# Performance work log

Measured on AMD Instinct MI355X. Metric: run time of the kernel, lower is better.

Reference implementation:

```python
import jax, jax.numpy as jnp
import numpy as np
from itertools import product


def _gen_exps(num_vars, degree):
    return [e for e in product(range(degree + 1), repeat=num_vars) if sum(e) <= degree]

EXP_W = _gen_exps(7, 3)  # 120 terms
EXP_B = _gen_exps(3, 3)  # 20 terms
EXP_M = _gen_exps(5, 3)  # 56 terms (+1 diagonal coeff)


def _powers(x, exps):
    return {e: x ** e for e in exps}


def setup_inputs() -> dict:
    key = jax.random.key(0)
    ks = jax.random.split(key, 12)
    B, Din, Dout = 65536, 64, 64
    return {
        'x1': jax.random.normal(ks[0], (B, Din), jnp.float32),
        's1': jax.random.normal(ks[1], (B, Dout), jnp.float32),
        'y1': jax.random.normal(ks[2], (B, Dout), jnp.float32),
        'x2': jax.random.normal(ks[3], (B, Din), jnp.float32),
        's2': jax.random.normal(ks[4], (B, Dout), jnp.float32),
        'y2': jax.random.normal(ks[5], (B, Dout), jnp.float32),
        'w': jax.random.normal(ks[6], (Dout, Din), jnp.float32) * 0.1,
        'b': jax.random.normal(ks[7], (Dout,), jnp.float32) * 0.1,
        'm': jax.random.normal(ks[8], (Dout, Dout), jnp.float32) * 0.1,
        'params_w': jax.random.normal(ks[9], (len(EXP_W),), jnp.float32) * 0.1,
        'params_b': jax.random.normal(ks[10], (len(EXP_B),), jnp.float32) * 0.1,
        'params_m': jax.random.normal(ks[11], (len(EXP_M) + 1,), jnp.float32) * 0.1,
    }


def _dw(x1, s1, y1, x2, s2, y2, w, params_w):
    px1 = _powers(x1, {e[0] for e in EXP_W})
    ps1 = _powers(s1, {e[1] for e in EXP_W})
    py1 = _powers(y1, {e[2] for e in EXP_W})
    px2 = _powers(x2, {e[3] for e in EXP_W})
    ps2 = _powers(s2, {e[4] for e in EXP_W})
    py2 = _powers(y2, {e[5] for e in EXP_W})
    pw = _powers(w, {e[6] for e in EXP_W})
    inv_b = 1.0 / x1.shape[0]
    delta_w = jnp.zeros_like(w)
    for i, e in enumerate(EXP_W):
        y_term = ps1[e[1]] * py1[e[2]] * ps2[e[4]] * py2[e[5]]  # [B, Dout]
        x_term = px1[e[0]] * px2[e[3]]                          # [B, Din]
        delta_w = delta_w + (params_w[i] * inv_b) * (y_term.T @ x_term) * pw[e[6]]
    return delta_w  # bound=None (identity), l2_reg=0


def _db(y1, y2, b, params_b):
    py1 = _powers(y1, {e[0] for e in EXP_B})
    py2 = _powers(y2, {e[1] for e in EXP_B})
    pb = _powers(b, {e[2] for e in EXP_B})
    inv_b = 1.0 / y1.shape[0]
    delta_b = jnp.zeros_like(b)
    for i, e in enumerate(EXP_B):
        delta_b = delta_b + (params_b[i] * inv_b) * jnp.sum(py1[e[0]] * py2[e[1]], axis=0) * pb[e[2]]
    return delta_b


def _dm(y1, y2, m, params_m):
    ey1 = {e[0] for e in EXP_M} | {e[1] for e in EXP_M}
    ey2 = {e[2] for e in EXP_M} | {e[3] for e in EXP_M}
    py1 = _powers(y1, ey1)
    py2 = _powers(y2, ey2)
    pm = _powers(m, {e[4] for e in EXP_M})
    inv_b = 1.0 / y1.shape[0]
    delta_m = jnp.zeros_like(m)
    for i, e in enumerate(EXP_M):
        left = py1[e[1]] * py2[e[3]]   # [B, Dout]
        right = py1[e[0]] * py2[e[2]]  # [B, Dout]
        delta_m = delta_m + (params_m[i] * inv_b) * (left.T @ right) * pm[e[4]]
    delta_m = delta_m + params_m[-1] * jnp.eye(m.shape[0], dtype=m.dtype)
    return delta_m


def reference(x1, s1, y1, x2, s2, y2, w, b, m, params_w, params_b, params_m):
    delta_w = _dw(x1, s1, y1, x2, s2, y2, w, params_w)
    delta_b = _db(y1, y2, b, params_b)
    delta_m = _dm(y1, y2, m, params_m)
    return delta_w, delta_b, delta_m
```

## Files before the change

kernel.cpp:

```cpp
#include <hip/hip_runtime.h>
#include <type_traits>
#include <stdint.h>

#define DEV __device__ __forceinline__

typedef float f32x4 __attribute__((ext_vector_type(4)));
typedef short bf16x8 __attribute__((ext_vector_type(8)));
typedef unsigned short u16;
typedef u16 u16x4 __attribute__((ext_vector_type(4)));

static constexpr int BTOT = 65536;
static constexpr int KB   = 64;
static constexpr int NCHT = BTOT / KB;
static constexpr int NG   = 56;
static constexpr int NCOLSUM = 45;
static constexpr float INVB = 1.0f / (float)BTOT;

static constexpr int NWIN  = 32;
static constexpr int CHW   = NCHT / NWIN;
static constexpr int NCOLG = 7;
static constexpr int GRID  = 8*NWIN;
static constexpr int BUFHALF = 8*4096;

struct Col {
  int nslot, np;
  int8_t sexp[8][6];
  int8_t pa[8], pb[8];
  int16_t gout[8];
  uint8_t ldmask;
};

struct Tables {
  int nW, nB, nM, nA, nX;
  int8_t expw[120][7];
  int8_t expb[20][3];
  int8_t expm[56][5];
  int8_t am[35][4];
  int8_t xm[10][2];
  Col col[NCOLG];
  int8_t wtype[120]; int16_t widx[120]; int8_t wpow[120];
  int8_t mtype[56];  int16_t midx[56];  int8_t mpow[56];
  int16_t bcol[20];  int8_t bpow[20];
  int err, gcount;
};

constexpr int aidf(const Tables& t,int a,int b,int c,int d){
  for(int i=0;i<t.nA;i++)
    if(t.am[i][0]==a&&t.am[i][1]==b&&t.am[i][2]==c&&t.am[i][3]==d) return i;
  return -1;
}
constexpr int xidf(const Tables& t,int a,int b){
  for(int i=0;i<t.nX;i++) if(t.xm[i][0]==a&&t.xm[i][1]==b) return i;
  return -1;
}

constexpr Tables makeTables(){
  Tables t{};
  t.err = 0;
  t.nW=0;
  for(int e0=0;e0<4;e0++)for(int e1=0;e1<4;e1++)for(int e2=0;e2<4;e2++)
  for(int e3=0;e3<4;e3++)for(int e4=0;e4<4;e4++)for(int e5=0;e5<4;e5++)
  for(int e6=0;e6<4;e6++) if(e0+e1+e2+e3+e4+e5+e6<=3){
    t.expw[t.nW][0]=(int8_t)e0; t.expw[t.nW][1]=(int8_t)e1; t.expw[t.nW][2]=(int8_t)e2;
    t.expw[t.nW][3]=(int8_t)e3; t.expw[t.nW][4]=(int8_t)e4; t.expw[t.nW][5]=(int8_t)e5;
    t.expw[t.nW][6]=(int8_t)e6; t.nW++;
  }
  t.nB=0;
  for(int e0=0;e0<4;e0++)for(int e1=0;e1<4;e1++)for(int e2=0;e2<4;e2++)
    if(e0+e1+e2<=3){ t.expb[t.nB][0]=(int8_t)e0; t.expb[t.nB][1]=(int8_t)e1; t.expb[t.nB][2]=(int8_t)e2; t.nB++; }
  t.nM=0;
  for(int e0=0;e0<4;e0++)for(int e1=0;e1<4;e1++)for(int e2=0;e2<4;e2++)
  for(int e3=0;e3<4;e3++)for(int e4=0;e4<4;e4++)
    if(e0+e1+e2+e3+e4<=3){
      t.expm[t.nM][0]=(int8_t)e0; t.expm[t.nM][1]=(int8_t)e1; t.expm[t.nM][2]=(int8_t)e2;
      t.expm[t.nM][3]=(int8_t)e3; t.expm[t.nM][4]=(int8_t)e4; t.nM++;
    }
  t.nA=0;
  for(int a=0;a<4;a++)for(int b=0;b<4;b++)for(int c=0;c<4;c++)for(int d=0;d<4;d++)
    if(a+b+c+d<=3){ t.am[t.nA][0]=(int8_t)a; t.am[t.nA][1]=(int8_t)b; t.am[t.nA][2]=(int8_t)c; t.am[t.nA][3]=(int8_t)d; t.nA++; }
  t.nX=0;
  for(int a=0;a<4;a++)for(int b=0;b<4;b++)
    if(a+b<=3){ t.xm[t.nX][0]=(int8_t)a; t.xm[t.nX][1]=(int8_t)b; t.nX++; }

  int wslot[35][10]; int mslot[10][10];
  for(int i=0;i<35;i++)for(int j=0;j<10;j++) wslot[i][j]=-1;
  for(int i=0;i<10;i++)for(int j=0;j<10;j++) mslot[i][j]=-1;

  int slot=0;

  {
    Col& c=t.col[0]; c.nslot=4; c.np=8;
    int ym[4][2]={{0,1},{1,0},{0,2},{1,1}};
    for(int s=0;s<4;s++){ for(int q=0;q<6;q++)c.sexp[s][q]=0;
      c.sexp[s][1]=(int8_t)ym[s][0]; c.sexp[s][3]=(int8_t)ym[s][1]; }
    int p=0;
    for(int L=0;L<2;L++)for(int R=0;R<4;R++){
      c.pa[p]=(int8_t)L; c.pb[p]=(int8_t)R; c.gout[p]=(int16_t)slot;
      mslot[xidf(t,ym[L][0],ym[L][1])][xidf(t,ym[R][0],ym[R][1])]=slot; slot++; p++;
    }
  }
  {
    Col& c=t.col[1]; c.nslot=5; c.np=8;
    int ym[5][2]={{0,1},{1,0},{0,2},{1,1},{2,0}};
    for(int s=0;s<5;s++){ for(int q=0;q<6;q++)c.sexp[s][q]=0;
      c.sexp[s][1]=(int8_t)ym[s][0]; c.sexp[s][3]=(int8_t)ym[s][1]; }
    int p=0;
    for(int L=0;L<2;L++){
      c.pa[p]=(int8_t)L; c.pb[p]=4; c.gout[p]=(int16_t)slot;
      mslot[xidf(t,ym[L][0],ym[L][1])][xidf(t,2,0)]=slot; slot++; p++;
    }
    for(int i=0;i<3;i++)for(int j=0;j<2;j++){
      c.pa[p]=(int8_t)(2+i); c.pb[p]=(int8_t)j; c.gout[p]=(int16_t)slot;
      mslot[xidf(t,ym[2+i][0],ym[2+i][1])][xidf(t,ym[j][0],ym[j][1])]=slot; slot++; p++;
    }
  }
  for(int wc=0; wc<2; wc++){
    Col& c=t.col[2+2*wc]; c.nslot=6; c.np=8;
    int am2[2][2]={{1,0},{0,1}};
    int xb[4][2]={{0,1},{1,0},{0,2},{1,1}};
    for(int s=0;s<6;s++) for(int q=0;q<6;q++) c.sexp[s][q]=0;
    for(int s=0;s<2;s++){
      c.sexp[s][wc?2:0]=(int8_t)am2[s][0]; c.sexp[s][wc?3:1]=(int8_t)am2[s][1];
    }
    for(int s=0;s<4;s++){ c.sexp[2+s][4]=(int8_t)xb[s][0]; c.sexp[2+s][5]=(int8_t)xb[s][1]; }
    int p=0;
    for(int a=0;a<2;a++)for(int b=0;b<4;b++){
      int amid = wc? aidf(t,0,0,am2[a][0],am2[a][1]) : aidf(t,am2[a][0],am2[a][1],0,0);
      if(amid<0) t.err+=1;
      c.pa[p]=(int8_t)a; c.pb[p]=(int8_t)(2+b); c.gout[p]=(int16_t)slot;
      wslot[amid][xidf(t,xb[b][0],xb[b][1])]=slot; slot++; p++;
    }
  }
  for(int wc=0; wc<2; wc++){
    Col& c=t.col[3+2*wc]; c.nslot=8; c.np=8;
    int am5[5][2]={{1,0},{0,1},{2,0},{1,1},{0,2}};
    int xb[3][2]={{2,0},{0,1},{1,0}};
    for(int s=0;s<8;s++) for(int q=0;q<6;q++) c.sexp[s][q]=0;
    for(int s=0;s<5;s++){
      c.sexp[s][wc?2:0]=(int8_t)am5[s][0]; c.sexp[s][wc?3:1]=(int8_t)am5[s][1];
    }
    for(int s=0;s<3;s++){ c.sexp[5+s][4]=(int8_t)xb[s][0]; c.sexp[5+s][5]=(int8_t)xb[s][1]; }
    int p=0;
    for(int a=0;a<2;a++){
      int amid = wc? aidf(t,0,0,am5[a][0],am5[a][1]) : aidf(t,am5[a][0],am5[a][1],0,0);
      if(amid<0) t.err+=1;
      c.pa[p]=(int8_t)a; c.pb[p]=5; c.gout[p]=(int16_t)slot;
      wslot[amid][xidf(t,2,0)]=slot; slot++; p++;
    }
    for(int i=0;i<3;i++)for(int j=0;j<2;j++){
      int amid = wc? aidf(t,0,0,am5[2+i][0],am5[2+i][1]) : aidf(t,am5[2+i][0],am5[2+i][1],0,0);
      if(amid<0) t.err+=1;
      c.pa[p]=(int8_t)(2+i); c.pb[p]=(int8_t)(6+j); c.gout[p]=(int16_t)slot;
      wslot[amid][xidf(t,xb[1+j][0],xb[1+j][1])]=slot; slot++; p++;
    }
  }
  {
    Col& c=t.col[6]; c.nslot=6; c.np=8;
    int a4[4][4]={{1,0,1,0},{1,0,0,1},{0,1,1,0},{0,1,0,1}};
    int xb[2][2]={{0,1},{1,0}};
    for(int s=0;s<6;s++) for(int q=0;q<6;q++) c.sexp[s][q]=0;
    for(int s=0;s<4;s++) for(int q=0;q<4;q++) c.sexp[s][q]=(int8_t)a4[s][q];
    for(int s=0;s<2;s++){ c.sexp[4+s][4]=(int8_t)xb[s][0]; c.sexp[4+s][5]=(int8_t)xb[s][1]; }
    int p=0;
    for(int a=0;a<4;a++)for(int b=0;b<2;b++){
      int amid = aidf(t,a4[a][0],a4[a][1],a4[a][2],a4[a][3]);
      if(amid<0) t.err+=1;
      c.pa[p]=(int8_t)a; c.pb[p]=(int8_t)(4+b); c.gout[p]=(int16_t)slot;
      wslot[amid][xidf(t,xb[b][0],xb[b][1])]=slot; slot++; p++;
    }
  }
  t.gcount=slot;
  if(slot!=NG) t.err+=1;

  for(int ci=0; ci<NCOLG; ci++){
    unsigned m=0;
    for(int s=0;s<t.col[ci].nslot;s++)
      for(int v=0;v<6;v++) if(t.col[ci].sexp[s][v]>0) m |= (1u<<v);
    t.col[ci].ldmask=(uint8_t)m;
  }

  for(int i=0;i<t.nW;i++){
    const int8_t* e=t.expw[i];
    bool u0=(e[0]==0&&e[3]==0);
    bool v0=(e[1]==0&&e[2]==0&&e[4]==0&&e[5]==0);
    t.wpow[i]=e[6];
    if(u0){ t.wtype[i]=1; t.widx[i]=(int16_t)aidf(t,e[1],e[2],e[4],e[5]); }
    else if(v0){ t.wtype[i]=2; t.widx[i]=(int16_t)xidf(t,e[0],e[3]); }
    else {
      int s=wslot[aidf(t,e[1],e[2],e[4],e[5])][xidf(t,e[0],e[3])];
      if(s<0) t.err+=1;
      t.wtype[i]=0; t.widx[i]=(int16_t)s;
    }
  }
  for(int i=0;i<t.nM;i++){
    const int8_t* e=t.expm[i];
    bool L0=(e[1]==0&&e[3]==0), R0=(e[0]==0&&e[2]==0);
    t.mpow[i]=e[4];
    if(L0){ t.mtype[i]=2; t.midx[i]=(int16_t)aidf(t,0,e[0],0,e[2]); }
    else if(R0){ t.mtype[i]=1; t.midx[i]=(int16_t)aidf(t,0,e[1],0,e[3]); }
    else {
      int s=mslot[xidf(t,e[1],e[3])][xidf(t,e[0],e[2])];
      if(s<0) t.err+=1;
      t.mtype[i]=0; t.midx[i]=(int16_t)s;
    }
  }
  for(int i=0;i<t.nB;i++){
    const int8_t* e=t.expb[i];
    t.bcol[i]=(int16_t)aidf(t,0,e[0],0,e[1]); t.bpow[i]=e[2];
  }
  return t;
}

constexpr Tables TB = makeTables();
static_assert(TB.err==0 && TB.gcount==56, "table build failed");
static_assert(TB.nW==120 && TB.nB==20 && TB.nM==56 && TB.nA==35 && TB.nX==10, "enumeration mismatch");

template<int N, typename F>
DEV void sunroll(F&& f){
  if constexpr (N > 0){
    sunroll<N-1>(static_cast<F&&>(f));
    f(std::integral_constant<int, N-1>{});
  }
}
template<int E> DEV float ipw(float x){
  if constexpr(E==0) return 1.0f;
  else if constexpr(E==1) return x;
  else if constexpr(E==2) return x*x;
  else return x*x*x;
}
DEV u16 f2bf(float f){
  uint32_t u = __builtin_bit_cast(uint32_t, f);
  u = u + 0x7FFFu + ((u>>16)&1u);
  return (u16)(u>>16);
}

DEV bf16x8 readFrag(const u16* L, int slot, int sb, int tt, int l){
  return *(const bf16x8*)&L[slot*4096 + ((sb*4 + tt)*64 + l)*8];
}
DEV f32x4 mfma_(bf16x8 a, bf16x8 b, f32x4 c){
  return __builtin_amdgcn_mfma_f32_16x16x32_bf16(a, b, c, 0, 0, 0);
}

template<int CI>
DEV void colGemm(const float* __restrict__ s1,const float* __restrict__ y1,
                 const float* __restrict__ s2,const float* __restrict__ y2,
                 const float* __restrict__ x1,const float* __restrict__ x2,
                 float* __restrict__ G, u16* lds, int tid, int bi)
{
  constexpr int NS = TB.col[CI].nslot;
  constexpr unsigned LM = TB.col[CI].ldmask;

  const int l = tid&63, w = tid>>6;
  const int wbase = ((w>>3)*4 + (l>>4))*512 + (((w>>1)&3)*16 + (l&15))*8 + (w&1)*4;

  const int c0 = bi*CHW, c1 = c0+CHW;
  f32x4 acc[4][2] = {};
  float rw[6][4] = {};

  auto issue = [&](int ck){
    const int b0 = (ck*KB + w*4)*64 + l;
    #pragma unroll
    for(int j=0;j<4;j++){
      const int off = b0 + j*64;
      if constexpr(LM&1u)  rw[0][j]=s1[off];
      if constexpr(LM&2u)  rw[1][j]=y1[off];
      if constexpr(LM&4u)  rw[2][j]=s2[off];
      if constexpr(LM&8u)  rw[3][j]=y2[off];
      if constexpr(LM&16u) rw[4][j]=x1[off];
      if constexpr(LM&32u) rw[5][j]=x2[off];
    }
  };
  auto stage = [&](int buf){
    u16* L = lds + buf*BUFHALF;
    sunroll<NS>([&](auto S){
      constexpr int s = decltype(S)::value;
      u16x4 o4;
      #pragma unroll
      for(int j=0;j<4;j++){
        float v = ipw<TB.col[CI].sexp[s][0]>(rw[0][j])
                * ipw<TB.col[CI].sexp[s][1]>(rw[1][j])
                * ipw<TB.col[CI].sexp[s][2]>(rw[2][j])
                * ipw<TB.col[CI].sexp[s][3]>(rw[3][j])
                * ipw<TB.col[CI].sexp[s][4]>(rw[4][j])
                * ipw<TB.col[CI].sexp[s][5]>(rw[5][j]);
        o4[j]=f2bf(v);
      }
      *(u16x4*)&L[s*4096 + wbase] = o4;
    });
  };

  issue(c0);
  stage(0);
  asm volatile("s_waitcnt lgkmcnt(0)" ::: "memory");
  __builtin_amdgcn_s_barrier();
  __builtin_amdgcn_sched_barrier(0);

  for(int k=c0; k<c1; ++k){
    const int t = k - c0;
    const bool notlast = (k+1 < c1);
    if(notlast) issue(k+1);

    const u16* L = lds + (t&1)*BUFHALF;
    sunroll<16>([&](auto WW){
      constexpr int ww = decltype(WW)::value;
      if(w==ww){
        constexpr int p  = ww>>1;
        constexpr int SA = TB.col[CI].pa[p];
        constexpr int SB = TB.col[CI].pb[p];
        constexpr int DB = (ww&1)*2;
        #pragma unroll
        for(int sb=0; sb<2; ++sb){
          bf16x8 Af[4];
          #pragma unroll
          for(int o2=0;o2<4;o2++) Af[o2]=readFrag(L,SA,sb,o2,l);
          #pragma unroll
          for(int dd=0;dd<2;dd++){
            bf16x8 Bf=readFrag(L,SB,sb,DB+dd,l);
            #pragma unroll
            for(int o2=0;o2<4;o2++) acc[o2][dd]=mfma_(Af[o2],Bf,acc[o2][dd]);
          }
        }
      }
    });

    if(notlast) stage((t+1)&1);

    asm volatile("s_waitcnt lgkmcnt(0)" ::: "memory");
    __builtin_amdgcn_s_barrier();
    __builtin_amdgcn_sched_barrier(0);
  }

  const int r0=(l>>4)*4, cc=l&15;
  sunroll<16>([&](auto WW){
    constexpr int ww = decltype(WW)::value;
    if(w==ww){
      constexpr int p  = ww>>1;
      constexpr int GS = TB.col[CI].gout[p];
      constexpr int DB = (ww&1)*2;
      float* dst = G + GS*4096;
      #pragma unroll
      for(int o2=0;o2<4;o2++)
        #pragma unroll
        for(int dd=0;dd<2;dd++)
          #pragma unroll
          for(int r=0;r<4;r++)
            atomicAdd(&dst[(o2*16+r0+r)*64 + (DB+dd)*16+cc], acc[o2][dd][r]);
    }
  });
}

DEV void colRed(const float* __restrict__ s1,const float* __restrict__ y1,
                const float* __restrict__ s2,const float* __restrict__ y2,
                const float* __restrict__ x1,const float* __restrict__ x2,
                float* __restrict__ col, float* ldsF, int tid, int bi)
{
  const int ch=tid&63, g16=tid>>6;
  const int base = bi*2048;
  float accv[45];
  sunroll<45>([&](auto K){ accv[decltype(K)::value]=0.f; });
  for(int r=base+g16; r<base+2048; r+=16){
    const int off=r*64+ch;
    const float v0=s1[off],v1=y1[off],v2=s2[off],v3=y2[off],v4=x1[off],v5=x2[off];
    sunroll<35>([&](auto K){
      constexpr int k=decltype(K)::value;
      accv[k] += ipw<TB.am[k][0]>(v0)*ipw<TB.am[k][1]>(v1)*ipw<TB.am[k][2]>(v2)*ipw<TB.am[k][3]>(v3);
    });
    sunroll<10>([&](auto K){
      constexpr int k=decltype(K)::value;
      accv[35+k] += ipw<TB.xm[k][0]>(v4)*ipw<TB.xm[k][1]>(v5);
    });
  }
  sunroll<6>([&](auto RR){
    constexpr int rr=decltype(RR)::value;
    __syncthreads();
    sunroll<8>([&](auto Q){
      constexpr int q=decltype(Q)::value;
      if constexpr(rr*8+q < 45)
        ldsF[(q*16+g16)*64+ch]=accv[rr*8+q];
    });
    __syncthreads();
    {
      const int k=tid>>6, c=tid&63;
      const int idx=rr*8+k;
      if(k<8 && idx<45){
        float s=0.f;
        #pragma unroll
        for(int gg=0; gg<16; gg++) s+=ldsF[(k*16+gg)*64+c];
        atomicAdd(&col[idx*64+c], s);
      }
    }
  });
}

__global__ __launch_bounds__(1024, 4) void k_main(
    const float* __restrict__ x1, const float* __restrict__ s1, const float* __restrict__ y1,
    const float* __restrict__ x2, const float* __restrict__ s2, const float* __restrict__ y2,
    float* __restrict__ G, float* __restrict__ col)
{
  __shared__ u16 lds[2*BUFHALF];
  const int tid = threadIdx.x;
  const int u = blockIdx.x >> 5;
  const int g = blockIdx.x & 31;
  if      (u==0) colGemm<0>(s1,y1,s2,y2,x1,x2,G,lds,tid,g);
  else if (u==1) colGemm<1>(s1,y1,s2,y2,x1,x2,G,lds,tid,g);
  else if (u==2) colGemm<2>(s1,y1,s2,y2,x1,x2,G,lds,tid,g);
  else if (u==3) colGemm<3>(s1,y1,s2,y2,x1,x2,G,lds,tid,g);
  else if (u==4) colGemm<4>(s1,y1,s2,y2,x1,x2,G,lds,tid,g);
  else if (u==5) colGemm<5>(s1,y1,s2,y2,x1,x2,G,lds,tid,g);
  else if (u==6) colGemm<6>(s1,y1,s2,y2,x1,x2,G,lds,tid,g);
  else           colRed(s1,y1,s2,y2,x1,x2,col,(float*)lds,tid,g);
}

__global__ __launch_bounds__(256) void k_combine(
    const float* __restrict__ G, const float* __restrict__ col,
    const float* __restrict__ w, const float* __restrict__ b, const float* __restrict__ m,
    const float* __restrict__ parw, const float* __restrict__ parb, const float* __restrict__ parm,
    float* __restrict__ out)
{
  const int n = blockIdx.x*256 + threadIdx.x;
  const int o = n>>6, d = n&63;
  const float wv = w[n], mv = m[n];
  const float wp[4] = {1.f, wv, wv*wv, wv*wv*wv};
  const float mp[4] = {1.f, mv, mv*mv, mv*mv*mv};
  float aw=0.f, am=0.f;
  sunroll<120>([&](auto II){
    constexpr int i = decltype(II)::value;
    constexpr int ty = TB.wtype[i];
    constexpr int ix = TB.widx[i];
    constexpr int q  = TB.wpow[i];
    float val;
    if constexpr(ty==0) val = G[ix*4096 + n];
    else if constexpr(ty==1) val = col[ix*64 + o];
    else val = col[(35+ix)*64 + d];
    aw += parw[i] * val * wp[q];
  });
  sunroll<56>([&](auto II){
    constexpr int i = decltype(II)::value;
    constexpr int ty = TB.mtype[i];
    constexpr int ix = TB.midx[i];
    constexpr int q  = TB.mpow[i];
    float val;
    if constexpr(ty==0) val = G[ix*4096 + n];
    else if constexpr(ty==1) val = col[ix*64 + o];
    else val = col[ix*64 + d];
    am += parm[i] * val * mp[q];
  });
  aw *= INVB; am *= INVB;
  if (o==d) am += parm[56];
  out[n] = aw;
  out[4160 + n] = am;
  if (n < 64){
    const float bv = b[n];
    const float bp[4] = {1.f, bv, bv*bv, bv*bv*bv};
    float ab=0.f;
    sunroll<20>([&](auto II){
      constexpr int i = decltype(II)::value;
      constexpr int cix = TB.bcol[i];
      constexpr int q = TB.bpow[i];
      ab += parb[i] * col[cix*64 + n] * bp[q];
    });
    out[4096 + n] = ab * INVB;
  }
}

extern "C" void kernel_launch(void* const* d_in, const int* in_sizes, int n_in,
                              void* d_out, int out_size, void* d_ws, size_t ws_size,
                              hipStream_t stream)
{
  const float* x1=(const float*)d_in[0];
  const float* s1=(const float*)d_in[1];
  const float* y1=(const float*)d_in[2];
  const float* x2=(const float*)d_in[3];
  const float* s2=(const float*)d_in[4];
  const float* y2=(const float*)d_in[5];
  const float* w =(const float*)d_in[6];
  const float* b =(const float*)d_in[7];
  const float* m =(const float*)d_in[8];
  const float* parw=(const float*)d_in[9];
  const float* parb=(const float*)d_in[10];
  const float* parm=(const float*)d_in[11];

  float* G   = (float*)d_ws;
  float* col = G + NG*4096;

  hipMemsetAsync(d_ws, 0, (size_t)(NG*4096 + NCOLSUM*64)*sizeof(float), stream);
  k_main<<<GRID, 1024, 0, stream>>>(x1,s1,y1,x2,s2,y2,G,col);
  k_combine<<<16, 256, 0, stream>>>(G,col,w,b,m,parw,parb,parm,(float*)d_out);
}
```

Measured before the change: 97.11 us.

## Warp-specialize column GEMM into producer and MFMA consumer wavefronts

Splits the 16 wavefronts into 8 producers, which load inputs, compute the power products and write bf16 tiles to LDS, and 8 consumers, which run the MFMA chain for one full 64x64 product each. The consumers raise their scheduling priority. Previously every wave did both jobs in lockstep. The split aims to overlap global loads and elementwise work with the matrix math, and each consumer now owns a whole output tile. The cost is that each consumer holds a larger accumulator, 16 f32x4, which raises register pressure. Half the waves also never use the MFMA units, so throughput depends on the two groups staying balanced across barriers.

```diff
diff --git a/kernel.cpp b/kernel.cpp
--- a/kernel.cpp
+++ b/kernel.cpp
@@ -7,7 +7,7 @@
 typedef float f32x4 __attribute__((ext_vector_type(4)));
 typedef short bf16x8 __attribute__((ext_vector_type(8)));
 typedef unsigned short u16;
-typedef u16 u16x4 __attribute__((ext_vector_type(4)));
+typedef u16 u16x8 __attribute__((ext_vector_type(8)));
 
 static constexpr int BTOT = 65536;
 static constexpr int KB   = 64;
@@ -251,102 +251,102 @@
   constexpr unsigned LM = TB.col[CI].ldmask;
 
   const int l = tid&63, w = tid>>6;
-  const int wbase = ((w>>3)*4 + (l>>4))*512 + (((w>>1)&3)*16 + (l&15))*8 + (w&1)*4;
-
   const int c0 = bi*CHW, c1 = c0+CHW;
-  f32x4 acc[4][2] = {};
-  float rw[6][4] = {};
-
-  auto issue = [&](int ck){
-    const int b0 = (ck*KB + w*4)*64 + l;
-    #pragma unroll
-    for(int j=0;j<4;j++){
-      const int off = b0 + j*64;
-      if constexpr(LM&1u)  rw[0][j]=s1[off];
-      if constexpr(LM&2u)  rw[1][j]=y1[off];
-      if constexpr(LM&4u)  rw[2][j]=s2[off];
-      if constexpr(LM&8u)  rw[3][j]=y2[off];
-      if constexpr(LM&16u) rw[4][j]=x1[off];
-      if constexpr(LM&32u) rw[5][j]=x2[off];
-    }
-  };
-  auto stage = [&](int buf){
-    u16* L = lds + buf*BUFHALF;
-    sunroll<NS>([&](auto S){
-      constexpr int s = decltype(S)::value;
-      u16x4 o4;
+
+  if (w < 8){
+    const int pw = w;
+    const int wrbase = ((pw>>2)*4 + (l>>4))*512 + ((pw&3)*16 + (l&15))*8;
+    float rw[6][8];
+
+    auto LOAD = [&](int ck){
+      const int b0 = (ck*KB + pw*8)*64 + l;
       #pragma unroll
-      for(int j=0;j<4;j++){
-        float v = ipw<TB.col[CI].sexp[s][0]>(rw[0][j])
-                * ipw<TB.col[CI].sexp[s][1]>(rw[1][j])
-                * ipw<TB.col[CI].sexp[s][2]>(rw[2][j])
-                * ipw<TB.col[CI].sexp[s][3]>(rw[3][j])
-                * ipw<TB.col[CI].sexp[s][4]>(rw[4][j])
-                * ipw<TB.col[CI].sexp[s][5]>(rw[5][j]);
-        o4[j]=f2bf(v);
+      for(int j=0;j<8;j++){
+        const int off = b0 + j*64;
+        if constexpr(LM&1u)  rw[0][j]=s1[off];
+        if constexpr(LM&2u)  rw[1][j]=y1[off];
+        if constexpr(LM&4u)  rw[2][j]=s2[off];
+        if constexpr(LM&8u)  rw[3][j]=y2[off];
+        if constexpr(LM&16u) rw[4][j]=x1[off];
+        if constexpr(LM&32u) rw[5][j]=x2[off];
       }
-      *(u16x4*)&L[s*4096 + wbase] = o4;
-    });
-  };
-
-  issue(c0);
-  stage(0);
-  asm volatile("s_waitcnt lgkmcnt(0)" ::: "memory");
-  __builtin_amdgcn_s_barrier();
-  __builtin_amdgcn_sched_barrier(0);
-
-  for(int k=c0; k<c1; ++k){
-    const int t = k - c0;
-    const bool notlast = (k+1 < c1);
-    if(notlast) issue(k+1);
-
-    const u16* L = lds + (t&1)*BUFHALF;
-    sunroll<16>([&](auto WW){
-      constexpr int ww = decltype(WW)::value;
-      if(w==ww){
-        constexpr int p  = ww>>1;
-        constexpr int SA = TB.col[CI].pa[p];
-        constexpr int SB = TB.col[CI].pb[p];
-        constexpr int DB = (ww&1)*2;
+    };
+    auto PROD = [&](int buf){
+      u16* L = lds + buf*BUFHALF;
+      sunroll<NS>([&](auto S){
+        constexpr int s = decltype(S)::value;
+        u16x8 o8;
         #pragma unroll
-        for(int sb=0; sb<2; ++sb){
-          bf16x8 Af[4];
-          #pragma unroll
-          for(int o2=0;o2<4;o2++) Af[o2]=readFrag(L,SA,sb,o2,l);
-          #pragma unroll
-          for(int dd=0;dd<2;dd++){
-            bf16x8 Bf=readFrag(L,SB,sb,DB+dd,l);
-            #pragma unroll
-            for(int o2=0;o2<4;o2++) acc[o2][dd]=mfma_(Af[o2],Bf,acc[o2][dd]);
-          }
+        for(int j=0;j<8;j++){
+          float v = ipw<TB.col[CI].sexp[s][0]>(rw[0][j])
+                  * ipw<TB.col[CI].sexp[s][1]>(rw[1][j])
+                  * ipw<TB.col[CI].sexp[s][2]>(rw[2][j])
+                  * ipw<TB.col[CI].sexp[s][3]>(rw[3][j])
+                  * ipw<TB.col[CI].sexp[s][4]>(rw[4][j])
+                  * ipw<TB.col[CI].sexp[s][5]>(rw[5][j]);
+          o8[j]=f2bf(v);
         }
-      }
-    });
-
-    if(notlast) stage((t+1)&1);
-
+        *(u16x8*)&L[s*4096 + wrbase] = o8;
+      });
+    };
+
+    LOAD(c0); PROD(c0&1);
     asm volatile("s_waitcnt lgkmcnt(0)" ::: "memory");
     __builtin_amdgcn_s_barrier();
     __builtin_amdgcn_sched_barrier(0);
-  }
-
-  const int r0=(l>>4)*4, cc=l&15;
-  sunroll<16>([&](auto WW){
-    constexpr int ww = decltype(WW)::value;
-    if(w==ww){
-      constexpr int p  = ww>>1;
-      constexpr int GS = TB.col[CI].gout[p];
-      constexpr int DB = (ww&1)*2;
-      float* dst = G + GS*4096;
+
+    for(int k=c0; k<c1; ++k){
+      if(k+1 < c1){ LOAD(k+1); PROD((k+1)&1); }
+      asm volatile("s_waitcnt lgkmcnt(0)" ::: "memory");
+      __builtin_amdgcn_s_barrier();
+      __builtin_amdgcn_sched_barrier(0);
+    }
+  } else {
+    int aslot=0, bslot=0, gsl=0;
+    sunroll<8>([&](auto PP){
+      constexpr int p = decltype(PP)::value;
+      if(w == 8+p){
+        aslot = TB.col[CI].pa[p];
+        bslot = TB.col[CI].pb[p];
+        gsl   = TB.col[CI].gout[p];
+      }
+    });
+    f32x4 acc[4][4] = {};
+
+    __builtin_amdgcn_s_barrier();
+    __builtin_amdgcn_sched_barrier(0);
+
+    for(int k=c0; k<c1; ++k){
+      const u16* L = lds + (k&1)*BUFHALF;
+      __builtin_amdgcn_s_setprio(1);
       #pragma unroll
-      for(int o2=0;o2<4;o2++)
+      for(int sb=0; sb<2; ++sb){
+        bf16x8 Af[4];
         #pragma unroll
-        for(int dd=0;dd<2;dd++)
+        for(int o2=0;o2<4;o2++) Af[o2]=readFrag(L,aslot,sb,o2,l);
+        #pragma unroll
+        for(int dd=0;dd<4;dd++){
+          bf16x8 Bf=readFrag(L,bslot,sb,dd,l);
           #pragma unroll
-          for(int r=0;r<4;r++)
-            atomicAdd(&dst[(o2*16+r0+r)*64 + (DB+dd)*16+cc], acc[o2][dd][r]);
-    }
-  });
+          for(int o2=0;o2<4;o2++) acc[o2][dd]=mfma_(Af[o2],Bf,acc[o2][dd]);
+        }
+      }
+      __builtin_amdgcn_s_setprio(0);
+      asm volatile("s_waitcnt lgkmcnt(0)" ::: "memory");
+      __builtin_amdgcn_s_barrier();
+      __builtin_amdgcn_sched_barrier(0);
+    }
+
+    const int r0=(l>>4)*4, cc=l&15;
+    float* dst = G + gsl*4096;
+    #pragma unroll
+    for(int o2=0;o2<4;o2++)
+      #pragma unroll
+      for(int dd=0;dd<4;dd++)
+        #pragma unroll
+        for(int r=0;r<4;r++)
+          atomicAdd(&dst[(o2*16+r0+r)*64 + dd*16+cc], acc[o2][dd][r]);
+  }
 }
 
 DEV void colRed(const float* __restrict__ s1,const float* __restrict__ y1,
```

Result: slower. 107.7 us (+10.9%).

## Remap staging thread-to-element layout and replace per-wave unrolled dispatch with runtime slots

Applied to the files above, without the earlier changes.

Each thread now loads a different (channel, batch) element from global memory and writes its packed bf16 values contiguously at tid*4 in LDS, so the LDS stores are linear. The fragment layout read by MFMA is unchanged. The 16-way compile-time per-wave branch, in both the MFMA loop and the atomic epilogue, is replaced by runtime slot indices chosen once. This shrinks code size and instruction-cache pressure. The cost is less coalesced global loads and dynamic LDS addressing instead of constant offsets.

```diff
diff --git a/kernel.cpp b/kernel.cpp
--- a/kernel.cpp
+++ b/kernel.cpp
@@ -251,14 +251,29 @@
   constexpr unsigned LM = TB.col[CI].ldmask;
 
   const int l = tid&63, w = tid>>6;
-  const int wbase = ((w>>3)*4 + (l>>4))*512 + (((w>>1)&3)*16 + (l&15))*8 + (w&1)*4;
+  const int P = tid>>7, Q = (tid>>1)&63, h = tid&1;
+  const int chS = (P&3)*16 + (Q&15);
+  const int bS  = (P>>2)*32 + (Q>>4)*8 + h*4;
+  const int wbase = tid*4;
+
+  int aslot=0,bslot=0,gsl=0,dbase=0;
+  sunroll<16>([&](auto W){
+    constexpr int ww = decltype(W)::value;
+    if(w==ww){
+      constexpr int p = ww>>1;
+      aslot = TB.col[CI].pa[p];
+      bslot = TB.col[CI].pb[p];
+      gsl   = TB.col[CI].gout[p];
+      dbase = (ww&1)*2;
+    }
+  });
 
   const int c0 = bi*CHW, c1 = c0+CHW;
   f32x4 acc[4][2] = {};
   float rw[6][4] = {};
 
   auto issue = [&](int ck){
-    const int b0 = (ck*KB + w*4)*64 + l;
+    const int b0 = (ck*KB + bS)*64 + chS;
     #pragma unroll
     for(int j=0;j<4;j++){
       const int off = b0 + j*64;
@@ -301,27 +316,18 @@
     if(notlast) issue(k+1);
 
     const u16* L = lds + (t&1)*BUFHALF;
-    sunroll<16>([&](auto WW){
-      constexpr int ww = decltype(WW)::value;
-      if(w==ww){
-        constexpr int p  = ww>>1;
-        constexpr int SA = TB.col[CI].pa[p];
-        constexpr int SB = TB.col[CI].pb[p];
-        constexpr int DB = (ww&1)*2;
+    #pragma unroll
+    for(int sb=0; sb<2; ++sb){
+      bf16x8 Af[4];
+      #pragma unroll
+      for(int o2=0;o2<4;o2++) Af[o2]=readFrag(L,aslot,sb,o2,l);
+      #pragma unroll
+      for(int dd=0;dd<2;dd++){
+        bf16x8 Bf=readFrag(L,bslot,sb,dbase+dd,l);
         #pragma unroll
-        for(int sb=0; sb<2; ++sb){
-          bf16x8 Af[4];
-          #pragma unroll
-          for(int o2=0;o2<4;o2++) Af[o2]=readFrag(L,SA,sb,o2,l);
-          #pragma unroll
-          for(int dd=0;dd<2;dd++){
-            bf16x8 Bf=readFrag(L,SB,sb,DB+dd,l);
-            #pragma unroll
-            for(int o2=0;o2<4;o2++) acc[o2][dd]=mfma_(Af[o2],Bf,acc[o2][dd]);
-          }
-        }
+        for(int o2=0;o2<4;o2++) acc[o2][dd]=mfma_(Af[o2],Bf,acc[o2][dd]);
       }
-    });
+    }
 
     if(notlast) stage((t+1)&1);
 
@@ -331,22 +337,14 @@
   }
 
   const int r0=(l>>4)*4, cc=l&15;
-  sunroll<16>([&](auto WW){
-    constexpr int ww = decltype(WW)::value;
-    if(w==ww){
-      constexpr int p  = ww>>1;
-      constexpr int GS = TB.col[CI].gout[p];
-      constexpr int DB = (ww&1)*2;
-      float* dst = G + GS*4096;
+  float* dst = G + gsl*4096;
+  #pragma unroll
+  for(int o2=0;o2<4;o2++)
+    #pragma unroll
+    for(int dd=0;dd<2;dd++)
       #pragma unroll
-      for(int o2=0;o2<4;o2++)
-        #pragma unroll
-        for(int dd=0;dd<2;dd++)
-          #pragma unroll
-          for(int r=0;r<4;r++)
-            atomicAdd(&dst[(o2*16+r0+r)*64 + (DB+dd)*16+cc], acc[o2][dd][r]);
-    }
-  });
+      for(int r=0;r<4;r++)
+        atomicAdd(&dst[(o2*16+r0+r)*64 + (dbase+dd)*16+cc], acc[o2][dd][r]);
 }
 
 DEV void colRed(const float* __restrict__ s1,const float* __restrict__ y1,
```

After: 127.7 us. 1.31x slower.
